# Kernel tuning notes

Measured on AMD Instinct MI355X. Metric: run time of the kernel, lower is better.

Reference implementation:

```python
import jax, jax.numpy as jnp
import numpy as np

N_FEATURES = 26          # number of feature categories (FEATURE_AND_ENCODER entries)
VOCAB_PER_FEATURE = 50000  # ids in [f*V, (f+1)*V) belong to feature f
SLOTS_PER_FEATURE = 8
BATCH = 16384
EMBED = 32
VOCAB = N_FEATURES * VOCAB_PER_FEATURE


def setup_inputs() -> dict:
    key = jax.random.key(0)
    ks = jax.random.split(key, 8)
    P = N_FEATURES * SLOTS_PER_FEATURE  # 208 ids per row
    x = jax.random.randint(ks[0], (BATCH, P), 0, VOCAB, dtype=jnp.int64)
    table = jax.random.normal(ks[1], (VOCAB, EMBED), dtype=jnp.float32) * 0.1
    D = N_FEATURES * EMBED  # 832
    W0 = jax.random.normal(ks[2], (D, 64), dtype=jnp.float32) * (1.0 / np.sqrt(D))
    b0 = jax.random.normal(ks[3], (64,), dtype=jnp.float32) * 0.01
    W1 = jax.random.normal(ks[4], (64, 16), dtype=jnp.float32) * (1.0 / 8.0)
    b1 = jax.random.normal(ks[5], (16,), dtype=jnp.float32) * 0.01
    W2 = jax.random.normal(ks[6], (16, 1), dtype=jnp.float32) * 0.25
    return {"x": x, "table": table, "W0": W0, "b0": b0, "W1": W1, "b1": b1, "W2": W2}


def reference(x, table, W0, b0, W1, b1, W2):
    B = x.shape[0]
    # dynamic embedding lookup: [B, P, E]
    embeds = table[x]
    # category of each id (what encoder.match_category encodes): [B, P]
    cat = x // VOCAB_PER_FEATURE
    # mask+gather+reduce_sum per feature == one-hot segment sum over features
    onehot = jax.nn.one_hot(cat, N_FEATURES, dtype=table.dtype)  # [B, P, F]
    pooled = jnp.einsum('bpe,bpf->bfe', embeds, onehot)          # [B, F, E]
    feats = pooled.reshape(B, N_FEATURES * EMBED)                # concat of per-feature sums
    h = jax.nn.relu(feats @ W0 + b0)
    h = jax.nn.relu(h @ W1 + b1)
    logits = h @ W2
    return jax.nn.sigmoid(logits)
```

## Files before the change

kernel.cpp:

```cpp
#include <hip/hip_runtime.h>
#include <math.h>

#define BATCH 16384
#define PP    208
#define NF    26
#define VPF   50000u
#define EMB   32
#define DD    832

typedef __attribute__((ext_vector_type(8))) short short8v;
typedef __attribute__((ext_vector_type(4))) float float4v;

static __device__ __forceinline__ ushort f32_to_bf16(float f) {
    unsigned u = __builtin_bit_cast(unsigned, f);
    unsigned r = (u + 0x7fffu + ((u >> 16) & 1u)) >> 16;
    return (ushort)r;
}

__global__ __launch_bounds__(256) void prep_kernel(const float* __restrict__ W0,
                                                   ushort* __restrict__ w0p) {
    const int i = blockIdx.x * 256 + threadIdx.x;
    if (i < DD * 64) {
        const int k = i >> 6, c = i & 63;
        const int kt = k >> 5, kk = k & 31;
        w0p[(kt * 64 + c) * 32 + kk] = f32_to_bf16(W0[i]);
    }
}

__global__ __launch_bounds__(256, 8) void pool_kernel(const int* __restrict__ x,
                                                      const float* __restrict__ table,
                                                      ushort* __restrict__ feats) {
    __shared__ int   s_ids[PP];
    __shared__ float s_pool[DD];

    const int    tid = threadIdx.x;
    const size_t row = blockIdx.x;

    for (int i = tid; i < DD; i += 256) s_pool[i] = 0.0f;
    if (tid < PP) s_ids[tid] = x[row * PP + tid];
    __syncthreads();

    const int e  = tid & 31;
    const int p0 = (tid >> 5) * 26;
    float* pool  = s_pool + e;

#pragma unroll 1
    for (int b = 0; b < 24; b += 4) {
        const unsigned id0 = (unsigned)s_ids[p0 + b + 0];
        const unsigned id1 = (unsigned)s_ids[p0 + b + 1];
        const unsigned id2 = (unsigned)s_ids[p0 + b + 2];
        const unsigned id3 = (unsigned)s_ids[p0 + b + 3];
        const float v0 = table[(size_t)id0 * EMB + e];
        const float v1 = table[(size_t)id1 * EMB + e];
        const float v2 = table[(size_t)id2 * EMB + e];
        const float v3 = table[(size_t)id3 * EMB + e];
        atomicAdd(pool + (id0 / VPF) * EMB, v0);
        atomicAdd(pool + (id1 / VPF) * EMB, v1);
        atomicAdd(pool + (id2 / VPF) * EMB, v2);
        atomicAdd(pool + (id3 / VPF) * EMB, v3);
    }
    {
        const unsigned idA = (unsigned)s_ids[p0 + 24];
        const unsigned idB = (unsigned)s_ids[p0 + 25];
        const float vA = table[(size_t)idA * EMB + e];
        const float vB = table[(size_t)idB * EMB + e];
        atomicAdd(pool + (idA / VPF) * EMB, vA);
        atomicAdd(pool + (idB / VPF) * EMB, vB);
    }
    __syncthreads();

    if (tid < DD / 4) {
        ushort4 o;
        o.x = f32_to_bf16(s_pool[tid * 4 + 0]);
        o.y = f32_to_bf16(s_pool[tid * 4 + 1]);
        o.z = f32_to_bf16(s_pool[tid * 4 + 2]);
        o.w = f32_to_bf16(s_pool[tid * 4 + 3]);
        *reinterpret_cast<ushort4*>(feats + row * DD + tid * 4) = o;
    }
}

__global__ __launch_bounds__(256) void mlp_kernel(const ushort* __restrict__ feats,
                                                  const ushort* __restrict__ w0p,
                                                  const float* __restrict__ b0,
                                                  const float* __restrict__ W1,
                                                  const float* __restrict__ b1,
                                                  const float* __restrict__ W2,
                                                  float* __restrict__ out) {
    __shared__ float sH[64][65];
    __shared__ float sH1[64][17];

    const int tid   = threadIdx.x;
    const int wave  = tid >> 6;
    const int lane  = tid & 63;
    const int lrow  = lane & 15;
    const int lk    = lane >> 4;
    const int brow0 = blockIdx.x * 64;

    float4v acc[4];
#pragma unroll
    for (int n = 0; n < 4; ++n) acc[n] = (float4v){0.f, 0.f, 0.f, 0.f};

    const ushort* frow  = feats + (size_t)(brow0 + wave * 16 + lrow) * DD + lk * 8;
    const ushort* wbase = w0p + lrow * 32 + lk * 8;

#pragma unroll 2
    for (int kt = 0; kt < 26; ++kt) {
        const short8v a = *reinterpret_cast<const short8v*>(frow + kt * 32);
#pragma unroll
        for (int n = 0; n < 4; ++n) {
            const short8v b = *reinterpret_cast<const short8v*>(wbase + (size_t)(kt * 64 + n * 16) * 32);
            acc[n] = __builtin_amdgcn_mfma_f32_16x16x32_bf16(a, b, acc[n], 0, 0, 0);
        }
    }

#pragma unroll
    for (int n = 0; n < 4; ++n) {
        const int   col = n * 16 + lrow;
        const float bb  = b0[col];
#pragma unroll
        for (int r = 0; r < 4; ++r) {
            const int rr = wave * 16 + lk * 4 + r;
            sH[rr][col] = fmaxf(acc[n][r] + bb, 0.f);
        }
    }
    __syncthreads();

    {
        const int r = tid >> 2, cg = (tid & 3) * 4;
        float a0 = b1[cg + 0], a1 = b1[cg + 1], a2 = b1[cg + 2], a3 = b1[cg + 3];
#pragma unroll 8
        for (int k = 0; k < 64; ++k) {
            const float  h  = sH[r][k];
            const float4 wv = *reinterpret_cast<const float4*>(W1 + k * 16 + cg);
            a0 = fmaf(h, wv.x, a0);
            a1 = fmaf(h, wv.y, a1);
            a2 = fmaf(h, wv.z, a2);
            a3 = fmaf(h, wv.w, a3);
        }
        sH1[r][cg + 0] = fmaxf(a0, 0.f);
        sH1[r][cg + 1] = fmaxf(a1, 0.f);
        sH1[r][cg + 2] = fmaxf(a2, 0.f);
        sH1[r][cg + 3] = fmaxf(a3, 0.f);
    }
    __syncthreads();

    if (tid < 64) {
        float z = 0.f;
#pragma unroll
        for (int j = 0; j < 16; ++j) z = fmaf(sH1[tid][j], W2[j], z);
        out[brow0 + tid] = 1.f / (1.f + expf(-z));
    }
}

extern "C" void kernel_launch(void* const* d_in, const int* in_sizes, int n_in,
                              void* d_out, int out_size, void* d_ws, size_t ws_size,
                              hipStream_t stream) {
    const int*   x     = (const int*)d_in[0];
    const float* table = (const float*)d_in[1];
    const float* W0    = (const float*)d_in[2];
    const float* b0    = (const float*)d_in[3];
    const float* W1    = (const float*)d_in[4];
    const float* b1    = (const float*)d_in[5];
    const float* W2    = (const float*)d_in[6];
    float*       out   = (float*)d_out;

    ushort* feats16 = (ushort*)d_ws;
    ushort* w0p     = feats16 + (size_t)BATCH * DD;

    prep_kernel<<<(DD * 64 + 255) / 256, 256, 0, stream>>>(W0, w0p);
    pool_kernel<<<BATCH, 256, 0, stream>>>(x, table, feats16);
    mlp_kernel<<<BATCH / 64, 256, 0, stream>>>(feats16, w0p, b0, W1, b1, W2, out);
}
```

Measured before the change: 756.1 us.

## Store pooled features and W0 in MFMA fragment layout; shrink MLP tile to 16 rows

The pooling kernel now writes bf16 features straight into a pre-swizzled MFMA A-fragment layout, and W0 is pre-packed into per-wave B-fragment order. Both MLP operands can then be read as fully contiguous 16-byte lane loads. The MLP kernel now handles 16 rows per block, with each wave owning one 16-column slice and using two independent accumulators. The pooling kernel loads ids with int4 vectors, unrolls by 2 instead of 4, and lowers its occupancy hint from 8 to 4 blocks. This adds more MLP blocks, and the smaller unroll and occupancy hint in the gather-bound pool kernel could reduce memory-level parallelism.

```diff
diff --git a/kernel.cpp b/kernel.cpp
--- a/kernel.cpp
+++ b/kernel.cpp
@@ -7,6 +7,7 @@
 #define VPF   50000u
 #define EMB   32
 #define DD    832
+#define VOCAB (NF * 50000)
 
 typedef __attribute__((ext_vector_type(8))) short short8v;
 typedef __attribute__((ext_vector_type(4))) float float4v;
@@ -16,20 +17,28 @@
     unsigned r = (u + 0x7fffu + ((u >> 16) & 1u)) >> 16;
     return (ushort)r;
 }
+static __device__ __forceinline__ unsigned pack_bf16x2(float lo, float hi) {
+    return (unsigned)f32_to_bf16(lo) | ((unsigned)f32_to_bf16(hi) << 16);
+}
 
-__global__ __launch_bounds__(256) void prep_kernel(const float* __restrict__ W0,
-                                                   ushort* __restrict__ w0p) {
+
+__global__ __launch_bounds__(256) void prep_w0(const float* __restrict__ W0,
+                                               ushort* __restrict__ w0p) {
     const int i = blockIdx.x * 256 + threadIdx.x;
     if (i < DD * 64) {
-        const int k = i >> 6, c = i & 63;
-        const int kt = k >> 5, kk = k & 31;
-        w0p[(kt * 64 + c) * 32 + kk] = f32_to_bf16(W0[i]);
+        const int j    = i & 7;
+        const int lane = (i >> 3) & 63;
+        const int w    = (i >> 9) & 3;
+        const int kt   = i >> 11;
+        const int k    = kt * 32 + (lane >> 4) * 8 + j;
+        const int col  = w * 16 + (lane & 15);
+        w0p[i] = f32_to_bf16(W0[(size_t)k * 64 + col]);
     }
 }
 
-__global__ __launch_bounds__(256, 8) void pool_kernel(const int* __restrict__ x,
-                                                      const float* __restrict__ table,
-                                                      ushort* __restrict__ feats) {
+__global__ __launch_bounds__(256, 4) void pool_f32(const int* __restrict__ x,
+                                                   const float* __restrict__ table,
+                                                   ushort* __restrict__ featsw) {
     __shared__ int   s_ids[PP];
     __shared__ float s_pool[DD];
 
@@ -37,7 +46,9 @@
     const size_t row = blockIdx.x;
 
     for (int i = tid; i < DD; i += 256) s_pool[i] = 0.0f;
-    if (tid < PP) s_ids[tid] = x[row * PP + tid];
+    if (tid < PP / 4)
+        reinterpret_cast<int4*>(s_ids)[tid] =
+            reinterpret_cast<const int4*>(x + row * PP)[tid];
     __syncthreads();
 
     const int e  = tid & 31;
@@ -45,110 +56,88 @@
     float* pool  = s_pool + e;
 
 #pragma unroll 1
-    for (int b = 0; b < 24; b += 4) {
+    for (int b = 0; b < 26; b += 2) {
         const unsigned id0 = (unsigned)s_ids[p0 + b + 0];
         const unsigned id1 = (unsigned)s_ids[p0 + b + 1];
-        const unsigned id2 = (unsigned)s_ids[p0 + b + 2];
-        const unsigned id3 = (unsigned)s_ids[p0 + b + 3];
         const float v0 = table[(size_t)id0 * EMB + e];
         const float v1 = table[(size_t)id1 * EMB + e];
-        const float v2 = table[(size_t)id2 * EMB + e];
-        const float v3 = table[(size_t)id3 * EMB + e];
         atomicAdd(pool + (id0 / VPF) * EMB, v0);
         atomicAdd(pool + (id1 / VPF) * EMB, v1);
-        atomicAdd(pool + (id2 / VPF) * EMB, v2);
-        atomicAdd(pool + (id3 / VPF) * EMB, v3);
-    }
-    {
-        const unsigned idA = (unsigned)s_ids[p0 + 24];
-        const unsigned idB = (unsigned)s_ids[p0 + 25];
-        const float vA = table[(size_t)idA * EMB + e];
-        const float vB = table[(size_t)idB * EMB + e];
-        atomicAdd(pool + (idA / VPF) * EMB, vA);
-        atomicAdd(pool + (idB / VPF) * EMB, vB);
     }
     __syncthreads();
 
-    if (tid < DD / 4) {
-        ushort4 o;
-        o.x = f32_to_bf16(s_pool[tid * 4 + 0]);
-        o.y = f32_to_bf16(s_pool[tid * 4 + 1]);
-        o.z = f32_to_bf16(s_pool[tid * 4 + 2]);
-        o.w = f32_to_bf16(s_pool[tid * 4 + 3]);
-        *reinterpret_cast<ushort4*>(feats + row * DD + tid * 4) = o;
+    if (tid < 104) {
+        const int kt = tid >> 2;
+        const int lk = tid & 3;
+        const float* s = s_pool + kt * 32 + lk * 8;
+        uint4 o;
+        o.x = pack_bf16x2(s[0], s[1]);
+        o.y = pack_bf16x2(s[2], s[3]);
+        o.z = pack_bf16x2(s[4], s[5]);
+        o.w = pack_bf16x2(s[6], s[7]);
+        const size_t rb = row >> 4, lr = row & 15;
+        ushort* dst = featsw + (((rb * 26 + kt) * 64) + lk * 16 + lr) * 8;
+        *reinterpret_cast<uint4*>(dst) = o;
     }
 }
 
-__global__ __launch_bounds__(256) void mlp_kernel(const ushort* __restrict__ feats,
+__global__ __launch_bounds__(256) void mlp_kernel(const ushort* __restrict__ featsw,
                                                   const ushort* __restrict__ w0p,
                                                   const float* __restrict__ b0,
                                                   const float* __restrict__ W1,
                                                   const float* __restrict__ b1,
                                                   const float* __restrict__ W2,
                                                   float* __restrict__ out) {
-    __shared__ float sH[64][65];
-    __shared__ float sH1[64][17];
+    __shared__ float sH[16][65];
+    __shared__ float sH1[16][17];
 
-    const int tid   = threadIdx.x;
-    const int wave  = tid >> 6;
-    const int lane  = tid & 63;
-    const int lrow  = lane & 15;
-    const int lk    = lane >> 4;
-    const int brow0 = blockIdx.x * 64;
+    const int tid  = threadIdx.x;
+    const int w    = tid >> 6;
+    const int lane = tid & 63;
+    const int rb   = blockIdx.x;
 
-    float4v acc[4];
+    const ushort* A = featsw + ((size_t)rb * 26 * 64 + lane) * 8;
+    const ushort* B = w0p + (size_t)(w * 64 + lane) * 8;
+
+    float4v acc0 = (float4v){0.f, 0.f, 0.f, 0.f};
+    float4v acc1 = (float4v){0.f, 0.f, 0.f, 0.f};
+
 #pragma unroll
-    for (int n = 0; n < 4; ++n) acc[n] = (float4v){0.f, 0.f, 0.f, 0.f};
-
-    const ushort* frow  = feats + (size_t)(brow0 + wave * 16 + lrow) * DD + lk * 8;
-    const ushort* wbase = w0p + lrow * 32 + lk * 8;
-
-#pragma unroll 2
-    for (int kt = 0; kt < 26; ++kt) {
-        const short8v a = *reinterpret_cast<const short8v*>(frow + kt * 32);
-#pragma unroll
-        for (int n = 0; n < 4; ++n) {
-            const short8v b = *reinterpret_cast<const short8v*>(wbase + (size_t)(kt * 64 + n * 16) * 32);
-            acc[n] = __builtin_amdgcn_mfma_f32_16x16x32_bf16(a, b, acc[n], 0, 0, 0);
-        }
+    for (int kt = 0; kt < 26; kt += 2) {
+        const short8v a0 = *reinterpret_cast<const short8v*>(A + (size_t)kt * 512);
+        const short8v b0v = *reinterpret_cast<const short8v*>(B + (size_t)kt * 2048);
+        const short8v a1 = *reinterpret_cast<const short8v*>(A + (size_t)(kt + 1) * 512);
+        const short8v b1v = *reinterpret_cast<const short8v*>(B + (size_t)(kt + 1) * 2048);
+        acc0 = __builtin_amdgcn_mfma_f32_16x16x32_bf16(a0, b0v, acc0, 0, 0, 0);
+        acc1 = __builtin_amdgcn_mfma_f32_16x16x32_bf16(a1, b1v, acc1, 0, 0, 0);
     }
 
-#pragma unroll
-    for (int n = 0; n < 4; ++n) {
-        const int   col = n * 16 + lrow;
+    {
+        const int   col = w * 16 + (lane & 15);
         const float bb  = b0[col];
 #pragma unroll
         for (int r = 0; r < 4; ++r) {
-            const int rr = wave * 16 + lk * 4 + r;
-            sH[rr][col] = fmaxf(acc[n][r] + bb, 0.f);
+            const int rr = (lane >> 4) * 4 + r;
+            sH[rr][col] = fmaxf(acc0[r] + acc1[r] + bb, 0.f);
         }
     }
     __syncthreads();
 
     {
-        const int r = tid >> 2, cg = (tid & 3) * 4;
-        float a0 = b1[cg + 0], a1 = b1[cg + 1], a2 = b1[cg + 2], a3 = b1[cg + 3];
+        const int r = tid >> 4, c = tid & 15;
+        float a0 = b1[c];
 #pragma unroll 8
-        for (int k = 0; k < 64; ++k) {
-            const float  h  = sH[r][k];
-            const float4 wv = *reinterpret_cast<const float4*>(W1 + k * 16 + cg);
-            a0 = fmaf(h, wv.x, a0);
-            a1 = fmaf(h, wv.y, a1);
-            a2 = fmaf(h, wv.z, a2);
-            a3 = fmaf(h, wv.w, a3);
-        }
-        sH1[r][cg + 0] = fmaxf(a0, 0.f);
-        sH1[r][cg + 1] = fmaxf(a1, 0.f);
-        sH1[r][cg + 2] = fmaxf(a2, 0.f);
-        sH1[r][cg + 3] = fmaxf(a3, 0.f);
+        for (int k = 0; k < 64; ++k)
+            a0 = fmaf(sH[r][k], W1[k * 16 + c], a0);
+        sH1[r][c] = fmaxf(a0, 0.f);
     }
     __syncthreads();
 
-    if (tid < 64) {
+    if (tid < 16) {
         float z = 0.f;
 #pragma unroll
         for (int j = 0; j < 16; ++j) z = fmaf(sH1[tid][j], W2[j], z);
-        out[brow0 + tid] = 1.f / (1.f + expf(-z));
+        out[(size_t)rb * 16 + tid] = 1.f / (1.f + expf(-z));
     }
 }
 
@@ -164,10 +153,10 @@
     const float* W2    = (const float*)d_in[6];
     float*       out   = (float*)d_out;
 
-    ushort* feats16 = (ushort*)d_ws;
-    ushort* w0p     = feats16 + (size_t)BATCH * DD;
+    ushort* featsw = (ushort*)d_ws;
+    ushort* w0p    = featsw + (size_t)BATCH * DD;
 
-    prep_kernel<<<(DD * 64 + 255) / 256, 256, 0, stream>>>(W0, w0p);
-    pool_kernel<<<BATCH, 256, 0, stream>>>(x, table, feats16);
-    mlp_kernel<<<BATCH / 64, 256, 0, stream>>>(feats16, w0p, b0, W1, b1, W2, out);
+    prep_w0<<<(DD * 64 + 255) / 256, 256, 0, stream>>>(W0, w0p);
+    pool_f32<<<BATCH, 256, 0, stream>>>(x, table, featsw);
+    mlp_kernel<<<BATCH / 16, 256, 0, stream>>>(featsw, w0p, b0, W1, b1, W2, out);
 }
```

Measured after the change: 744.2 us. No clear change (-1.6%).
